# Performance work log

Hardware: AMD Instinct MI355X
Metric: run time of the kernel (lower is better)

The kernel has to match this reference:

```python
import jax, jax.numpy as jnp
import numpy as np

INPUT_DIM, LATENT_DIM, HIDDEN_DIM = 256, 128, 256
B, S = 1024, 256


def _linear_params(key, fan_in, fan_out):
    kw, kb = jax.random.split(key)
    scale = 1.0 / np.sqrt(fan_in)
    W = jax.random.uniform(kw, (fan_in, fan_out), jnp.float32, -scale, scale)
    b = jax.random.uniform(kb, (fan_out,), jnp.float32, -scale, scale)
    return W, b


def setup_inputs() -> dict:
    key = jax.random.key(0)
    ks = jax.random.split(key, 9)
    enc = jax.random.normal(ks[0], (B, S, INPUT_DIM), jnp.float32)
    prev_latent = jax.random.normal(ks[1], (B, LATENT_DIM), jnp.float32)
    eps = jax.random.normal(ks[2], (B, S, LATENT_DIM), jnp.float32)
    pW1, pb1 = _linear_params(ks[3], INPUT_DIM + LATENT_DIM, HIDDEN_DIM)
    pW2, pb2 = _linear_params(ks[4], HIDDEN_DIM, HIDDEN_DIM)
    pW3, pb3 = _linear_params(ks[5], HIDDEN_DIM, 2 * LATENT_DIM)
    qW1, qb1 = _linear_params(ks[6], 2 * INPUT_DIM + LATENT_DIM, HIDDEN_DIM)
    qW2, qb2 = _linear_params(ks[7], HIDDEN_DIM, HIDDEN_DIM)
    qW3, qb3 = _linear_params(ks[8], HIDDEN_DIM, 2 * LATENT_DIM)
    return {
        "encoder_features": enc, "prev_latent": prev_latent, "eps": eps,
        "pW1": pW1, "pb1": pb1, "pW2": pW2, "pb2": pb2, "pW3": pW3, "pb3": pb3,
        "qW1": qW1, "qb1": qb1, "qW2": qW2, "qb2": qb2, "qW3": qW3, "qb3": qb3,
    }


def _mlp3(x, W1, b1, W2, b2, W3, b3):
    h = jax.nn.relu(x @ W1 + b1)
    h = jax.nn.relu(h @ W2 + b2)
    return h @ W3 + b3


def reference(encoder_features, prev_latent, eps,
              pW1, pb1, pW2, pb2, pW3, pb3,
              qW1, qb1, qW2, qb2, qW3, qb3):
    # time-major for scan: [S, B, D]
    h_seq = jnp.swapaxes(encoder_features, 0, 1)
    e_seq = jnp.swapaxes(eps, 0, 1)

    def step(z, xs):
        h_t, e_t = xs  # [B, input_dim], [B, latent_dim]
        prior_out = _mlp3(jnp.concatenate([h_t, z], -1), pW1, pb1, pW2, pb2, pW3, pb3)
        pm, plv = jnp.split(prior_out, 2, axis=-1)
        post_out = _mlp3(jnp.concatenate([h_t, z, h_t], -1), qW1, qb1, qW2, qb2, qW3, qb3)
        qm, qlv = jnp.split(post_out, 2, axis=-1)
        z_t = qm + e_t * jnp.exp(0.5 * qlv)  # reparameterization
        return z_t, (z_t, pm, plv, qm, qlv)

    _, (z, pm, plv, qm, qlv) = jax.lax.scan(step, prev_latent, (h_seq, e_seq))
    # back to batch-major [B, S, latent_dim]
    tb = lambda a: jnp.swapaxes(a, 0, 1)
    return tb(z), tb(pm), tb(plv), tb(qm), tb(qlv)
```

## Files before the change

### kernel.cpp

```cpp
#include <hip/hip_runtime.h>


typedef __attribute__((ext_vector_type(8))) short bfrag8;
typedef __attribute__((ext_vector_type(4))) float facc4;
typedef __attribute__((ext_vector_type(4))) unsigned int u32x4;

__device__ __forceinline__ unsigned short f2bf(float x) {
  unsigned int u = __float_as_uint(x);
  u = (u + 0x7fffu + ((u >> 16) & 1u)) >> 16;
  return (unsigned short)u;
}
__device__ __forceinline__ unsigned int pk2(float a, float b) {
  return (unsigned int)f2bf(a) | ((unsigned int)f2bf(b) << 16);
}
__device__ __forceinline__ float bf2f(unsigned int lo) {
  return __uint_as_float(lo << 16);
}
__device__ __forceinline__ facc4 mfma_bf16(bfrag8 a, bfrag8 b, facc4 c) {
  return __builtin_amdgcn_mfma_f32_16x16x32_bf16(a, b, c, 0, 0, 0);
}
__device__ __forceinline__ bfrag8 load_pin(const unsigned short* p) {
  u32x4 v = *(const u32x4*)p;
  asm volatile("" : "+v"(v));
  return __builtin_bit_cast(bfrag8, v);
}
__device__ __forceinline__ void wg_barrier() {
  asm volatile("s_waitcnt lgkmcnt(0)" ::: "memory");
  __builtin_amdgcn_sched_barrier(0);
  __builtin_amdgcn_s_barrier();
  __builtin_amdgcn_sched_barrier(0);
}
#define SWC(r, c) ((c) ^ (((r) & 8) << 1))

__global__ void pack_all(const float* __restrict__ qW1, const float* __restrict__ qW2,
                         const float* __restrict__ qW3, const float* __restrict__ pW1,
                         const float* __restrict__ pW2, const float* __restrict__ pW3,
                         unsigned short* __restrict__ ws) {
  int b = blockIdx.x;
  const float* src; const float* src2 = nullptr; unsigned short* dst; int KT;
  if (b < 32)       { src = qW1; src2 = qW1 + 384 * 256; dst = ws;          KT = 8; }
  else if (b < 48)  { b -= 32;  src = qW1 + 256 * 256;   dst = ws + 65536;  KT = 4; }
  else if (b < 80)  { b -= 48;  src = qW2;               dst = ws + 98304;  KT = 8; }
  else if (b < 112) { b -= 80;  src = qW3;               dst = ws + 163840; KT = 8; }
  else if (b < 144) { b -= 112; src = pW1;               dst = ws + 229376; KT = 8; }
  else if (b < 160) { b -= 144; src = pW1 + 256 * 256;   dst = ws + 294912; KT = 4; }
  else if (b < 192) { b -= 160; src = pW2;               dst = ws + 327680; KT = 8; }
  else              { b -= 192; src = pW3;               dst = ws + 393216; KT = 8; }
  int t = b * 256 + (int)threadIdx.x;
  if (t >= 16 * KT * 64) return;
  int l  = t & 63;
  int kt = (t >> 6) % KT;
  int nt = t / (64 * KT);
  int n  = nt * 16 + (l & 15);
  int k0 = kt * 32 + (l >> 4) * 8;
  unsigned int o[4];
#pragma unroll
  for (int p = 0; p < 4; ++p) {
    float a = src[(size_t)(k0 + 2 * p) * 256 + n];
    float c = src[(size_t)(k0 + 2 * p + 1) * 256 + n];
    if (src2) {
      a += src2[(size_t)(k0 + 2 * p) * 256 + n];
      c += src2[(size_t)(k0 + 2 * p + 1) * 256 + n];
    }
    o[p] = pk2(a, c);
  }
  *(uint4*)(dst + (size_t)t * 8) = make_uint4(o[0], o[1], o[2], o[3]);
}

__global__ __launch_bounds__(256, 2) void k1_pre(
    const float* __restrict__ enc, const unsigned short* __restrict__ wq,
    const unsigned short* __restrict__ wp, const float* __restrict__ qb1,
    unsigned short* __restrict__ cq, unsigned short* __restrict__ cp) {
  __shared__ unsigned short xl[32 * 264];
  const int bid = blockIdx.x;
  const int gp = bid >> 8, s = bid & 255;
  const int tid = threadIdx.x;
  {
    int row = tid >> 3, c0 = (tid & 7) * 32;
    const float* sp = enc + (((size_t)(gp * 32 + row) * 256 + s) * 256 + c0);
#pragma unroll
    for (int q = 0; q < 4; ++q) {
      float4 a = *(const float4*)(sp + q * 8);
      float4 b = *(const float4*)(sp + q * 8 + 4);
      *(uint4*)(&xl[row * 264 + SWC(row, c0 + q * 8)]) =
          make_uint4(pk2(a.x, a.y), pk2(a.z, a.w), pk2(b.x, b.y), pk2(b.z, b.w));
    }
  }
  __syncthreads();
  const int w = tid >> 6, l = tid & 63, lm = l & 15, lg = l >> 4;
  const int rr = lg * 4;
  const int nt[4] = {2 * w, 2 * w + 1, 2 * w + 8, 2 * w + 9};
  facc4 aq[2][4], ap[2][4];
#pragma unroll
  for (int j = 0; j < 4; ++j) {
    float bv = qb1[nt[j] * 16 + lm];
    aq[0][j] = (facc4){bv, bv, bv, bv}; aq[1][j] = aq[0][j];
    ap[0][j] = (facc4){0.f, 0.f, 0.f, 0.f}; ap[1][j] = ap[0][j];
  }
#pragma unroll
  for (int kt = 0; kt < 8; ++kt) {
    bfrag8 bq[4], bp[4];
#pragma unroll
    for (int j = 0; j < 4; ++j) {
      bq[j] = *(const bfrag8*)(wq + ((size_t)(nt[j] * 8 + kt) * 64 + l) * 8);
      bp[j] = *(const bfrag8*)(wp + ((size_t)(nt[j] * 8 + kt) * 64 + l) * 8);
    }
#pragma unroll
    for (int rt = 0; rt < 2; ++rt) {
      bfrag8 x = *(const bfrag8*)(&xl[(rt * 16 + lm) * 264 + SWC(lm, kt * 32 + lg * 8)]);
#pragma unroll
      for (int j = 0; j < 4; ++j) {
        aq[rt][j] = mfma_bf16(x, bq[j], aq[rt][j]);
        ap[rt][j] = mfma_bf16(x, bp[j], ap[rt][j]);
      }
    }
  }
#pragma unroll
  for (int rt = 0; rt < 2; ++rt) {
    size_t base = ((size_t)((gp * 2 + rt) * 256 + s)) * 512 + (size_t)tid * 2;
    ((uint4*)cq)[base + 0] =
        make_uint4(pk2(aq[rt][0][0], aq[rt][0][1]), pk2(aq[rt][0][2], aq[rt][0][3]),
                   pk2(aq[rt][2][0], aq[rt][2][1]), pk2(aq[rt][2][2], aq[rt][2][3]));
    ((uint4*)cq)[base + 1] =
        make_uint4(pk2(aq[rt][1][0], aq[rt][1][1]), pk2(aq[rt][1][2], aq[rt][1][3]),
                   pk2(aq[rt][3][0], aq[rt][3][1]), pk2(aq[rt][3][2], aq[rt][3][3]));
#pragma unroll
    for (int i = 0; i < 4; ++i) {
      int b = gp * 32 + rt * 16 + rr + i;
      ((uint2*)cp)[((size_t)b * 256 + s) * 64 + w * 16 + lm] =
          make_uint2(pk2(ap[rt][0][i], ap[rt][1][i]), pk2(ap[rt][2][i], ap[rt][3][i]));
    }
  }
}

__global__ __launch_bounds__(512, 2) void k2_scan(
    const float* __restrict__ prevz, const float* __restrict__ eps,
    const unsigned short* __restrict__ wU, const unsigned short* __restrict__ wW2,
    const unsigned short* __restrict__ wW3,
    const float* __restrict__ qb2, const float* __restrict__ qb3,
    const unsigned short* __restrict__ cq,
    float* __restrict__ z_o, float* __restrict__ qm_o, float* __restrict__ qlv_o) {
  __shared__ unsigned short zl[16 * 136];
  __shared__ unsigned short h1[16 * 264];
  __shared__ unsigned short h2[16 * 264];
  const int g = blockIdx.x, tid = threadIdx.x;
  const int w = tid >> 6, l = tid & 63, lm = l & 15, lg = l >> 4;
  const int rr = lg * 4;
  const int c = 16 * w + lm;
  const int cc[2] = {c, 128 + c};

  bfrag8 u[2][4], w2[2][8], w3[2][8];
#pragma unroll
  for (int j = 0; j < 2; ++j) {
    const int nt = w + 8 * j;
#pragma unroll
    for (int kt = 0; kt < 4; ++kt)
      u[j][kt] = load_pin(wU + ((size_t)(nt * 4 + kt) * 64 + l) * 8);
#pragma unroll
    for (int kt = 0; kt < 8; ++kt) {
      w2[j][kt] = load_pin(wW2 + ((size_t)(nt * 8 + kt) * 64 + l) * 8);
      w3[j][kt] = load_pin(wW3 + ((size_t)(nt * 8 + kt) * 64 + l) * 8);
    }
  }
  const float b2[2] = {qb2[c], qb2[128 + c]};
  const float b3[2] = {qb3[c], qb3[128 + c]};
  {
    int row = tid >> 5, q0 = (tid & 31) * 4;
    float4 v = *(const float4*)(prevz + (size_t)(g * 16 + row) * 128 + q0);
    *(uint2*)(&zl[row * 136 + SWC(row, q0)]) = make_uint2(pk2(v.x, v.y), pk2(v.z, v.w));
  }
  const uint4* cqp = (const uint4*)cq + ((size_t)g * 256) * 512 +
                     (size_t)((w >> 1) * 64 + l) * 2 + (w & 1);
  uint4 cb = cqp[0];
  float ep[4];
#pragma unroll
  for (int i = 0; i < 4; ++i)
    ep[i] = eps[((size_t)(g * 16 + rr + i) * 256) * 128 + c];
  __syncthreads();

  for (int s = 0; s < 256; ++s) {
    facc4 a[2];
    a[0][0] = bf2f(cb.x & 0xffffu); a[0][1] = bf2f(cb.x >> 16);
    a[0][2] = bf2f(cb.y & 0xffffu); a[0][3] = bf2f(cb.y >> 16);
    a[1][0] = bf2f(cb.z & 0xffffu); a[1][1] = bf2f(cb.z >> 16);
    a[1][2] = bf2f(cb.w & 0xffffu); a[1][3] = bf2f(cb.w >> 16);
    const int sn = (s + 1 < 256) ? s + 1 : s;
    const uint4 nb = cqp[(size_t)sn * 512];
    float epn[4];
#pragma unroll
    for (int i = 0; i < 4; ++i)
      epn[i] = eps[((size_t)(g * 16 + rr + i) * 256 + sn) * 128 + c];
#pragma unroll
    for (int kt = 0; kt < 4; ++kt) {
      bfrag8 zf = *(const bfrag8*)(&zl[lm * 136 + SWC(lm, kt * 32 + lg * 8)]);
      a[0] = mfma_bf16(zf, u[0][kt], a[0]);
      a[1] = mfma_bf16(zf, u[1][kt], a[1]);
    }
#pragma unroll
    for (int j = 0; j < 2; ++j)
#pragma unroll
      for (int i = 0; i < 4; ++i)
        h1[(rr + i) * 264 + SWC(rr + i, cc[j])] = f2bf(fmaxf(a[j][i], 0.f));
    wg_barrier();
    facc4 cv[2] = {(facc4){b2[0], b2[0], b2[0], b2[0]},
                   (facc4){b2[1], b2[1], b2[1], b2[1]}};
#pragma unroll
    for (int kt = 0; kt < 8; ++kt) {
      bfrag8 hf = *(const bfrag8*)(&h1[lm * 264 + SWC(lm, kt * 32 + lg * 8)]);
      cv[0] = mfma_bf16(hf, w2[0][kt], cv[0]);
      cv[1] = mfma_bf16(hf, w2[1][kt], cv[1]);
    }
#pragma unroll
    for (int j = 0; j < 2; ++j)
#pragma unroll
      for (int i = 0; i < 4; ++i)
        h2[(rr + i) * 264 + SWC(rr + i, cc[j])] = f2bf(fmaxf(cv[j][i], 0.f));
    wg_barrier();
    facc4 o[2] = {(facc4){b3[0], b3[0], b3[0], b3[0]},
                  (facc4){b3[1], b3[1], b3[1], b3[1]}};
#pragma unroll
    for (int kt = 0; kt < 8; ++kt) {
      bfrag8 hf = *(const bfrag8*)(&h2[lm * 264 + SWC(lm, kt * 32 + lg * 8)]);
      o[0] = mfma_bf16(hf, w3[0][kt], o[0]);
      o[1] = mfma_bf16(hf, w3[1][kt], o[1]);
    }
#pragma unroll
    for (int i = 0; i < 4; ++i) {
      size_t ob = ((size_t)(g * 16 + rr + i) * 256 + s) * 128;
      float zq = o[0][i] + ep[i] * __expf(0.5f * o[1][i]);
      qm_o[ob + c]  = o[0][i];
      qlv_o[ob + c] = o[1][i];
      z_o[ob + c]   = zq;
      zl[(rr + i) * 136 + SWC(rr + i, c)] = f2bf(zq);
    }
    wg_barrier();
    cb = nb;
#pragma unroll
    for (int i = 0; i < 4; ++i) ep[i] = epn[i];
  }
}

__global__ __launch_bounds__(256, 2) void k3_prior(
    const float* __restrict__ prevz, const float* __restrict__ z_in,
    const unsigned short* __restrict__ cp,
    const unsigned short* __restrict__ wU, const unsigned short* __restrict__ w2p,
    const unsigned short* __restrict__ w3p,
    const float* __restrict__ pb1, const float* __restrict__ pb2,
    const float* __restrict__ pb3,
    float* __restrict__ pm_o, float* __restrict__ plv_o) {
  __shared__ unsigned short zl[64 * 136];
  __shared__ unsigned short hb[64 * 264];
  const int bid = blockIdx.x;
  const int gp = bid >> 8, s = bid & 255;
  const int tid = threadIdx.x;
  const int w = tid >> 6, l = tid & 63, lm = l & 15, lg = l >> 4;
  const int rr = lg * 4;
  const int nt[4] = {2 * w, 2 * w + 1, 2 * w + 8, 2 * w + 9};
  const int c0 = 32 * w + lm, c1 = c0 + 16;
  const int cc[4] = {c0, c1, 128 + c0, 128 + c1};
  {
    int row = tid >> 2, q0 = (tid & 3) * 32;
    const float* sp = (s == 0) ? (prevz + (size_t)(gp * 64 + row) * 128 + q0)
                               : (z_in + ((size_t)(gp * 64 + row) * 256 + (s - 1)) * 128 + q0);
#pragma unroll
    for (int q = 0; q < 4; ++q) {
      float4 a = *(const float4*)(sp + q * 8);
      float4 b = *(const float4*)(sp + q * 8 + 4);
      *(uint4*)(&zl[row * 136 + SWC(row, q0 + q * 8)]) =
          make_uint4(pk2(a.x, a.y), pk2(a.z, a.w), pk2(b.x, b.y), pk2(b.z, b.w));
    }
  }
  const float pb[4] = {pb1[nt[0] * 16 + lm], pb1[nt[1] * 16 + lm],
                       pb1[nt[2] * 16 + lm], pb1[nt[3] * 16 + lm]};
  facc4 acc[4][4];
#pragma unroll
  for (int rt = 0; rt < 4; ++rt)
#pragma unroll
    for (int i = 0; i < 4; ++i) {
      int b = gp * 64 + rt * 16 + rr + i;
      uint2 v = ((const uint2*)cp)[((size_t)b * 256 + s) * 64 + w * 16 + lm];
      acc[rt][0][i] = pb[0] + bf2f(v.x & 0xffffu);
      acc[rt][1][i] = pb[1] + bf2f(v.x >> 16);
      acc[rt][2][i] = pb[2] + bf2f(v.y & 0xffffu);
      acc[rt][3][i] = pb[3] + bf2f(v.y >> 16);
    }
  __syncthreads();
#pragma unroll
  for (int kt = 0; kt < 4; ++kt) {
    bfrag8 b0 = *(const bfrag8*)(wU + ((size_t)(nt[0] * 4 + kt) * 64 + l) * 8);
    bfrag8 b1 = *(const bfrag8*)(wU + ((size_t)(nt[1] * 4 + kt) * 64 + l) * 8);
    bfrag8 b2f = *(const bfrag8*)(wU + ((size_t)(nt[2] * 4 + kt) * 64 + l) * 8);
    bfrag8 b3f = *(const bfrag8*)(wU + ((size_t)(nt[3] * 4 + kt) * 64 + l) * 8);
#pragma unroll
    for (int rt = 0; rt < 4; ++rt) {
      bfrag8 zf = *(const bfrag8*)(&zl[(rt * 16 + lm) * 136 + SWC(lm, kt * 32 + lg * 8)]);
      acc[rt][0] = mfma_bf16(zf, b0, acc[rt][0]);
      acc[rt][1] = mfma_bf16(zf, b1, acc[rt][1]);
      acc[rt][2] = mfma_bf16(zf, b2f, acc[rt][2]);
      acc[rt][3] = mfma_bf16(zf, b3f, acc[rt][3]);
    }
  }
#pragma unroll
  for (int rt = 0; rt < 4; ++rt)
#pragma unroll
    for (int j = 0; j < 4; ++j)
#pragma unroll
      for (int i = 0; i < 4; ++i) {
        int r = rt * 16 + rr + i;
        hb[r * 264 + SWC(r, cc[j])] = f2bf(fmaxf(acc[rt][j][i], 0.f));
      }
  __syncthreads();
  facc4 a2[4][4];
#pragma unroll
  for (int rt = 0; rt < 4; ++rt)
#pragma unroll
    for (int j = 0; j < 4; ++j) a2[rt][j] = (facc4){pb2[nt[j] * 16 + lm], pb2[nt[j] * 16 + lm],
                                                    pb2[nt[j] * 16 + lm], pb2[nt[j] * 16 + lm]};
#pragma unroll
  for (int kt = 0; kt < 8; ++kt) {
    bfrag8 b0 = *(const bfrag8*)(w2p + ((size_t)(nt[0] * 8 + kt) * 64 + l) * 8);
    bfrag8 b1 = *(const bfrag8*)(w2p + ((size_t)(nt[1] * 8 + kt) * 64 + l) * 8);
    bfrag8 b2f = *(const bfrag8*)(w2p + ((size_t)(nt[2] * 8 + kt) * 64 + l) * 8);
    bfrag8 b3f = *(const bfrag8*)(w2p + ((size_t)(nt[3] * 8 + kt) * 64 + l) * 8);
#pragma unroll
    for (int rt = 0; rt < 4; ++rt) {
      bfrag8 hf = *(const bfrag8*)(&hb[(rt * 16 + lm) * 264 + SWC(lm, kt * 32 + lg * 8)]);
      a2[rt][0] = mfma_bf16(hf, b0, a2[rt][0]);
      a2[rt][1] = mfma_bf16(hf, b1, a2[rt][1]);
      a2[rt][2] = mfma_bf16(hf, b2f, a2[rt][2]);
      a2[rt][3] = mfma_bf16(hf, b3f, a2[rt][3]);
    }
  }
  __syncthreads();
#pragma unroll
  for (int rt = 0; rt < 4; ++rt)
#pragma unroll
    for (int j = 0; j < 4; ++j)
#pragma unroll
      for (int i = 0; i < 4; ++i) {
        int r = rt * 16 + rr + i;
        hb[r * 264 + SWC(r, cc[j])] = f2bf(fmaxf(a2[rt][j][i], 0.f));
      }
  __syncthreads();
  facc4 a3[4][4];
#pragma unroll
  for (int rt = 0; rt < 4; ++rt)
#pragma unroll
    for (int j = 0; j < 4; ++j) a3[rt][j] = (facc4){pb3[nt[j] * 16 + lm], pb3[nt[j] * 16 + lm],
                                                    pb3[nt[j] * 16 + lm], pb3[nt[j] * 16 + lm]};
#pragma unroll
  for (int kt = 0; kt < 8; ++kt) {
    bfrag8 b0 = *(const bfrag8*)(w3p + ((size_t)(nt[0] * 8 + kt) * 64 + l) * 8);
    bfrag8 b1 = *(const bfrag8*)(w3p + ((size_t)(nt[1] * 8 + kt) * 64 + l) * 8);
    bfrag8 b2f = *(const bfrag8*)(w3p + ((size_t)(nt[2] * 8 + kt) * 64 + l) * 8);
    bfrag8 b3f = *(const bfrag8*)(w3p + ((size_t)(nt[3] * 8 + kt) * 64 + l) * 8);
#pragma unroll
    for (int rt = 0; rt < 4; ++rt) {
      bfrag8 hf = *(const bfrag8*)(&hb[(rt * 16 + lm) * 264 + SWC(lm, kt * 32 + lg * 8)]);
      a3[rt][0] = mfma_bf16(hf, b0, a3[rt][0]);
      a3[rt][1] = mfma_bf16(hf, b1, a3[rt][1]);
      a3[rt][2] = mfma_bf16(hf, b2f, a3[rt][2]);
      a3[rt][3] = mfma_bf16(hf, b3f, a3[rt][3]);
    }
  }
#pragma unroll
  for (int rt = 0; rt < 4; ++rt)
#pragma unroll
    for (int i = 0; i < 4; ++i) {
      size_t base = ((size_t)(gp * 64 + rt * 16 + rr + i) * 256 + s) * 128;
      pm_o[base + c0]  = a3[rt][0][i];
      pm_o[base + c1]  = a3[rt][1][i];
      plv_o[base + c0] = a3[rt][2][i];
      plv_o[base + c1] = a3[rt][3][i];
    }
}

extern "C" void kernel_launch(void* const* d_in, const int* in_sizes, int n_in,
                              void* d_out, int out_size, void* d_ws, size_t ws_size,
                              hipStream_t stream) {
  const float* enc   = (const float*)d_in[0];
  const float* prevz = (const float*)d_in[1];
  const float* eps   = (const float*)d_in[2];
  const float* pW1 = (const float*)d_in[3];
  const float* pb1 = (const float*)d_in[4];
  const float* pW2 = (const float*)d_in[5];
  const float* pb2 = (const float*)d_in[6];
  const float* pW3 = (const float*)d_in[7];
  const float* pb3 = (const float*)d_in[8];
  const float* qW1 = (const float*)d_in[9];
  const float* qb1 = (const float*)d_in[10];
  const float* qW2 = (const float*)d_in[11];
  const float* qb2 = (const float*)d_in[12];
  const float* qW3 = (const float*)d_in[13];
  const float* qb3 = (const float*)d_in[14];

  float* out = (float*)d_out;
  const size_t O = (size_t)1024 * 256 * 128;
  float* z_o   = out;
  float* pm_o  = out + O;
  float* plv_o = out + 2 * O;
  float* qm_o  = out + 3 * O;
  float* qlv_o = out + 4 * O;
  unsigned short* cq = (unsigned short*)pm_o;
  unsigned short* cp = (unsigned short*)plv_o;

  unsigned short* ws = (unsigned short*)d_ws;
  unsigned short* Wqe  = ws;
  unsigned short* Uq   = ws + 65536;
  unsigned short* W2q  = ws + 98304;
  unsigned short* W3q  = ws + 163840;
  unsigned short* W1ph = ws + 229376;
  unsigned short* Up   = ws + 294912;
  unsigned short* W2p  = ws + 327680;
  unsigned short* W3p  = ws + 393216;

  pack_all<<<224, 256, 0, stream>>>(qW1, qW2, qW3, pW1, pW2, pW3, ws);
  k1_pre<<<8192, 256, 0, stream>>>(enc, Wqe, W1ph, qb1, cq, cp);
  k2_scan<<<64, 512, 0, stream>>>(prevz, eps, Uq, W2q, W3q, qb2, qb3, cq,
                                  z_o, qm_o, qlv_o);
  k3_prior<<<4096, 256, 0, stream>>>(prevz, z_o, cp, Up, W2p, W3p,
                                     pb1, pb2, pb3, pm_o, plv_o);
}
```

Measured before the change: 755.8 us.

## Fuse pre, scan and prior kernels into one persistent kernel with flag sync

```diff
diff --git a/kernel.cpp b/kernel.cpp
--- a/kernel.cpp
+++ b/kernel.cpp
@@ -4,6 +4,9 @@
 typedef __attribute__((ext_vector_type(8))) short bfrag8;
 typedef __attribute__((ext_vector_type(4))) float facc4;
 typedef __attribute__((ext_vector_type(4))) unsigned int u32x4;
+typedef unsigned long long ull;
+
+#define SCOPE_AGENT __HIP_MEMORY_SCOPE_AGENT
 
 __device__ __forceinline__ unsigned short f2bf(float x) {
   unsigned int u = __float_as_uint(x);
@@ -67,14 +70,12 @@
   *(uint4*)(dst + (size_t)t * 8) = make_uint4(o[0], o[1], o[2], o[3]);
 }
 
-__global__ __launch_bounds__(256, 2) void k1_pre(
+template<bool FUSED>
+__device__ __forceinline__ void k1_body(
+    int gp, int s, int tid, unsigned short* xl,
     const float* __restrict__ enc, const unsigned short* __restrict__ wq,
     const unsigned short* __restrict__ wp, const float* __restrict__ qb1,
-    unsigned short* __restrict__ cq, unsigned short* __restrict__ cp) {
-  __shared__ unsigned short xl[32 * 264];
-  const int bid = blockIdx.x;
-  const int gp = bid >> 8, s = bid & 255;
-  const int tid = threadIdx.x;
+    unsigned int* __restrict__ cq, unsigned short* __restrict__ cp) {
   {
     int row = tid >> 3, c0 = (tid & 7) * 32;
     const float* sp = enc + (((size_t)(gp * 32 + row) * 256 + s) * 256 + c0);
@@ -117,33 +118,38 @@
   }
 #pragma unroll
   for (int rt = 0; rt < 2; ++rt) {
-    size_t base = ((size_t)((gp * 2 + rt) * 256 + s)) * 512 + (size_t)tid * 2;
-    ((uint4*)cq)[base + 0] =
-        make_uint4(pk2(aq[rt][0][0], aq[rt][0][1]), pk2(aq[rt][0][2], aq[rt][0][3]),
-                   pk2(aq[rt][2][0], aq[rt][2][1]), pk2(aq[rt][2][2], aq[rt][2][3]));
-    ((uint4*)cq)[base + 1] =
-        make_uint4(pk2(aq[rt][1][0], aq[rt][1][1]), pk2(aq[rt][1][2], aq[rt][1][3]),
-                   pk2(aq[rt][3][0], aq[rt][3][1]), pk2(aq[rt][3][2], aq[rt][3][3]));
 #pragma unroll
     for (int i = 0; i < 4; ++i) {
       int b = gp * 32 + rt * 16 + rr + i;
-      ((uint2*)cp)[((size_t)b * 256 + s) * 64 + w * 16 + lm] =
-          make_uint2(pk2(ap[rt][0][i], ap[rt][1][i]), pk2(ap[rt][2][i], ap[rt][3][i]));
-    }
-  }
-}
-
-__global__ __launch_bounds__(512, 2) void k2_scan(
+      size_t rb = ((size_t)b * 256 + s) * 128;
+      unsigned int v0 = pk2(aq[rt][0][i], aq[rt][2][i]);
+      unsigned int v1 = pk2(aq[rt][1][i], aq[rt][3][i]);
+      ull vcp = (ull)pk2(ap[rt][0][i], ap[rt][1][i]) |
+                ((ull)pk2(ap[rt][2][i], ap[rt][3][i]) << 32);
+      size_t cpx = ((size_t)b * 256 + s) * 64 + w * 16 + lm;
+      if (FUSED) {
+        __hip_atomic_store(cq + rb + 32 * w + lm,      v0, __ATOMIC_RELAXED, SCOPE_AGENT);
+        __hip_atomic_store(cq + rb + 32 * w + 16 + lm, v1, __ATOMIC_RELAXED, SCOPE_AGENT);
+        __hip_atomic_store((ull*)cp + cpx, vcp, __ATOMIC_RELAXED, SCOPE_AGENT);
+      } else {
+        cq[rb + 32 * w + lm]      = v0;
+        cq[rb + 32 * w + 16 + lm] = v1;
+        ((ull*)cp)[cpx] = vcp;
+      }
+    }
+  }
+}
+
+template<bool FUSED>
+__device__ __forceinline__ void k2_body(
+    int g, int tid, unsigned short* zl, unsigned short* h1, unsigned short* h2,
     const float* __restrict__ prevz, const float* __restrict__ eps,
     const unsigned short* __restrict__ wU, const unsigned short* __restrict__ wW2,
     const unsigned short* __restrict__ wW3,
     const float* __restrict__ qb2, const float* __restrict__ qb3,
-    const unsigned short* __restrict__ cq,
-    float* __restrict__ z_o, float* __restrict__ qm_o, float* __restrict__ qlv_o) {
-  __shared__ unsigned short zl[16 * 136];
-  __shared__ unsigned short h1[16 * 264];
-  __shared__ unsigned short h2[16 * 264];
-  const int g = blockIdx.x, tid = threadIdx.x;
+    const unsigned int* __restrict__ cq,
+    float* __restrict__ z_o, float* __restrict__ qm_o, float* __restrict__ qlv_o,
+    int* cqflag, int* zdone) {
   const int w = tid >> 6, l = tid & 63, lm = l & 15, lg = l >> 4;
   const int rr = lg * 4;
   const int c = 16 * w + lm;
@@ -169,77 +175,326 @@
     float4 v = *(const float4*)(prevz + (size_t)(g * 16 + row) * 128 + q0);
     *(uint2*)(&zl[row * 136 + SWC(row, q0)]) = make_uint2(pk2(v.x, v.y), pk2(v.z, v.w));
   }
-  const uint4* cqp = (const uint4*)cq + ((size_t)g * 256) * 512 +
-                     (size_t)((w >> 1) * 64 + l) * 2 + (w & 1);
-  uint4 cb = cqp[0];
+  if (FUSED) {
+    if (tid == 0)
+      while (__hip_atomic_load(&cqflag[0], __ATOMIC_ACQUIRE, SCOPE_AGENT) < 32)
+        __builtin_amdgcn_s_sleep(2);
+    wg_barrier();
+  }
+  size_t rix[4];
+#pragma unroll
+  for (int i = 0; i < 4; ++i)
+    rix[i] = ((size_t)(g * 16 + rr + i) * 256) * 128 + c;
+  unsigned int cb[4];
+#pragma unroll
+  for (int i = 0; i < 4; ++i) cb[i] = cq[rix[i]];
   float ep[4];
 #pragma unroll
   for (int i = 0; i < 4; ++i)
     ep[i] = eps[((size_t)(g * 16 + rr + i) * 256) * 128 + c];
   __syncthreads();
 
-  for (int s = 0; s < 256; ++s) {
-    facc4 a[2];
-    a[0][0] = bf2f(cb.x & 0xffffu); a[0][1] = bf2f(cb.x >> 16);
-    a[0][2] = bf2f(cb.y & 0xffffu); a[0][3] = bf2f(cb.y >> 16);
-    a[1][0] = bf2f(cb.z & 0xffffu); a[1][1] = bf2f(cb.z >> 16);
-    a[1][2] = bf2f(cb.w & 0xffffu); a[1][3] = bf2f(cb.w >> 16);
-    const int sn = (s + 1 < 256) ? s + 1 : s;
-    const uint4 nb = cqp[(size_t)sn * 512];
-    float epn[4];
-#pragma unroll
-    for (int i = 0; i < 4; ++i)
-      epn[i] = eps[((size_t)(g * 16 + rr + i) * 256 + sn) * 128 + c];
-#pragma unroll
-    for (int kt = 0; kt < 4; ++kt) {
-      bfrag8 zf = *(const bfrag8*)(&zl[lm * 136 + SWC(lm, kt * 32 + lg * 8)]);
-      a[0] = mfma_bf16(zf, u[0][kt], a[0]);
-      a[1] = mfma_bf16(zf, u[1][kt], a[1]);
-    }
-#pragma unroll
-    for (int j = 0; j < 2; ++j)
+  for (int sb = 0; sb < 32; ++sb) {
+    if (FUSED) {
+      if (sb > 0 && l == 0)
+        __hip_atomic_fetch_add(&zdone[g], 1, __ATOMIC_RELEASE, SCOPE_AGENT);
+      if (tid == 0) {
+        int hi = sb * 8 + 8; if (hi > 255) hi = 255;
+        for (int q = sb * 8 + 1; q <= hi; ++q)
+          while (__hip_atomic_load(&cqflag[q], __ATOMIC_ACQUIRE, SCOPE_AGENT) < 32)
+            __builtin_amdgcn_s_sleep(2);
+      }
+      wg_barrier();
+    }
+#pragma unroll 1
+    for (int si = 0; si < 8; ++si) {
+      const int s = sb * 8 + si;
+      facc4 a[2];
+#pragma unroll
+      for (int i = 0; i < 4; ++i) {
+        a[0][i] = bf2f(cb[i] & 0xffffu);
+        a[1][i] = bf2f(cb[i] >> 16);
+      }
+      const int sn = (s + 1 < 256) ? s + 1 : s;
+      unsigned int nbv[4];
+#pragma unroll
+      for (int i = 0; i < 4; ++i) nbv[i] = cq[rix[i] + (size_t)sn * 128];
+      float epn[4];
 #pragma unroll
       for (int i = 0; i < 4; ++i)
-        h1[(rr + i) * 264 + SWC(rr + i, cc[j])] = f2bf(fmaxf(a[j][i], 0.f));
-    wg_barrier();
-    facc4 cv[2] = {(facc4){b2[0], b2[0], b2[0], b2[0]},
-                   (facc4){b2[1], b2[1], b2[1], b2[1]}};
-#pragma unroll
-    for (int kt = 0; kt < 8; ++kt) {
-      bfrag8 hf = *(const bfrag8*)(&h1[lm * 264 + SWC(lm, kt * 32 + lg * 8)]);
-      cv[0] = mfma_bf16(hf, w2[0][kt], cv[0]);
-      cv[1] = mfma_bf16(hf, w2[1][kt], cv[1]);
-    }
-#pragma unroll
-    for (int j = 0; j < 2; ++j)
-#pragma unroll
-      for (int i = 0; i < 4; ++i)
-        h2[(rr + i) * 264 + SWC(rr + i, cc[j])] = f2bf(fmaxf(cv[j][i], 0.f));
-    wg_barrier();
-    facc4 o[2] = {(facc4){b3[0], b3[0], b3[0], b3[0]},
-                  (facc4){b3[1], b3[1], b3[1], b3[1]}};
-#pragma unroll
-    for (int kt = 0; kt < 8; ++kt) {
-      bfrag8 hf = *(const bfrag8*)(&h2[lm * 264 + SWC(lm, kt * 32 + lg * 8)]);
-      o[0] = mfma_bf16(hf, w3[0][kt], o[0]);
-      o[1] = mfma_bf16(hf, w3[1][kt], o[1]);
-    }
+        epn[i] = eps[((size_t)(g * 16 + rr + i) * 256 + sn) * 128 + c];
+#pragma unroll
+      for (int kt = 0; kt < 4; ++kt) {
+        bfrag8 zf = *(const bfrag8*)(&zl[lm * 136 + SWC(lm, kt * 32 + lg * 8)]);
+        a[0] = mfma_bf16(zf, u[0][kt], a[0]);
+        a[1] = mfma_bf16(zf, u[1][kt], a[1]);
+      }
+#pragma unroll
+      for (int j = 0; j < 2; ++j)
+#pragma unroll
+        for (int i = 0; i < 4; ++i)
+          h1[(rr + i) * 264 + SWC(rr + i, cc[j])] = f2bf(fmaxf(a[j][i], 0.f));
+      wg_barrier();
+      facc4 cv[2] = {(facc4){b2[0], b2[0], b2[0], b2[0]},
+                     (facc4){b2[1], b2[1], b2[1], b2[1]}};
+#pragma unroll
+      for (int kt = 0; kt < 8; ++kt) {
+        bfrag8 hf = *(const bfrag8*)(&h1[lm * 264 + SWC(lm, kt * 32 + lg * 8)]);
+        cv[0] = mfma_bf16(hf, w2[0][kt], cv[0]);
+        cv[1] = mfma_bf16(hf, w2[1][kt], cv[1]);
+      }
+#pragma unroll
+      for (int j = 0; j < 2; ++j)
+#pragma unroll
+        for (int i = 0; i < 4; ++i)
+          h2[(rr + i) * 264 + SWC(rr + i, cc[j])] = f2bf(fmaxf(cv[j][i], 0.f));
+      wg_barrier();
+      facc4 o[2] = {(facc4){b3[0], b3[0], b3[0], b3[0]},
+                    (facc4){b3[1], b3[1], b3[1], b3[1]}};
+#pragma unroll
+      for (int kt = 0; kt < 8; ++kt) {
+        bfrag8 hf = *(const bfrag8*)(&h2[lm * 264 + SWC(lm, kt * 32 + lg * 8)]);
+        o[0] = mfma_bf16(hf, w3[0][kt], o[0]);
+        o[1] = mfma_bf16(hf, w3[1][kt], o[1]);
+      }
+#pragma unroll
+      for (int i = 0; i < 4; ++i) {
+        size_t ob = ((size_t)(g * 16 + rr + i) * 256 + s) * 128;
+        float zq = o[0][i] + ep[i] * __expf(0.5f * o[1][i]);
+        qm_o[ob + c]  = o[0][i];
+        qlv_o[ob + c] = o[1][i];
+        if (FUSED)
+          __hip_atomic_store(&z_o[ob + c], zq, __ATOMIC_RELAXED, SCOPE_AGENT);
+        else
+          z_o[ob + c] = zq;
+        zl[(rr + i) * 136 + SWC(rr + i, c)] = f2bf(zq);
+      }
+      wg_barrier();
+#pragma unroll
+      for (int i = 0; i < 4; ++i) { cb[i] = nbv[i]; ep[i] = epn[i]; }
+    }
+  }
+  if (FUSED) {
+    asm volatile("s_waitcnt vmcnt(0)" ::: "memory");
+    if (l == 0)
+      __hip_atomic_fetch_add(&zdone[g], 1, __ATOMIC_RELEASE, SCOPE_AGENT);
+  }
+}
+
+template<bool FUSED>
+__device__ __forceinline__ void k3_body(
+    int gp, int s, int tid, unsigned short* zl, unsigned short* hb,
+    const float* __restrict__ prevz, const float* __restrict__ z_in,
+    const unsigned short* __restrict__ cp,
+    const unsigned short* __restrict__ wU, const unsigned short* __restrict__ w2p,
+    const unsigned short* __restrict__ w3p,
+    const float* __restrict__ pb1, const float* __restrict__ pb2,
+    const float* __restrict__ pb3,
+    float* __restrict__ pm_o, float* __restrict__ plv_o,
+    int* cqflag, int* zdone) {
+  if (FUSED) {
+    if (tid == 0) {
+      while (__hip_atomic_load(&cqflag[s], __ATOMIC_ACQUIRE, SCOPE_AGENT) < 32)
+        __builtin_amdgcn_s_sleep(8);
+      int need = 8 * ((s + 7) >> 3);
+      if (need) {
+#pragma unroll
+        for (int j = 0; j < 4; ++j)
+          while (__hip_atomic_load(&zdone[4 * gp + j], __ATOMIC_ACQUIRE, SCOPE_AGENT) < need)
+            __builtin_amdgcn_s_sleep(8);
+      }
+    }
+    __syncthreads();
+  }
+  const int w = tid >> 6, l = tid & 63, lm = l & 15, lg = l >> 4;
+  const int rr = lg * 4;
+  const int nt[4] = {2 * w, 2 * w + 1, 2 * w + 8, 2 * w + 9};
+  const int c0 = 32 * w + lm, c1 = c0 + 16;
+  const int cc[4] = {c0, c1, 128 + c0, 128 + c1};
+  {
+    int row = tid >> 2, q0 = (tid & 3) * 32;
+    const float* sp = (s == 0) ? (prevz + (size_t)(gp * 64 + row) * 128 + q0)
+                               : (z_in + ((size_t)(gp * 64 + row) * 256 + (s - 1)) * 128 + q0);
+#pragma unroll
+    for (int q = 0; q < 4; ++q) {
+      float4 a = *(const float4*)(sp + q * 8);
+      float4 b = *(const float4*)(sp + q * 8 + 4);
+      *(uint4*)(&zl[row * 136 + SWC(row, q0 + q * 8)]) =
+          make_uint4(pk2(a.x, a.y), pk2(a.z, a.w), pk2(b.x, b.y), pk2(b.z, b.w));
+    }
+  }
+  const float pb[4] = {pb1[nt[0] * 16 + lm], pb1[nt[1] * 16 + lm],
+                       pb1[nt[2] * 16 + lm], pb1[nt[3] * 16 + lm]};
+  facc4 acc[4][4];
+#pragma unroll
+  for (int rt = 0; rt < 4; ++rt)
 #pragma unroll
     for (int i = 0; i < 4; ++i) {
-      size_t ob = ((size_t)(g * 16 + rr + i) * 256 + s) * 128;
-      float zq = o[0][i] + ep[i] * __expf(0.5f * o[1][i]);
-      qm_o[ob + c]  = o[0][i];
-      qlv_o[ob + c] = o[1][i];
-      z_o[ob + c]   = zq;
-      zl[(rr + i) * 136 + SWC(rr + i, c)] = f2bf(zq);
-    }
-    wg_barrier();
-    cb = nb;
-#pragma unroll
-    for (int i = 0; i < 4; ++i) ep[i] = epn[i];
-  }
-}
-
+      int b = gp * 64 + rt * 16 + rr + i;
+      ull v = ((const ull*)cp)[((size_t)b * 256 + s) * 64 + w * 16 + lm];
+      unsigned int vx = (unsigned int)v, vy = (unsigned int)(v >> 32);
+      acc[rt][0][i] = pb[0] + bf2f(vx & 0xffffu);
+      acc[rt][1][i] = pb[1] + bf2f(vx >> 16);
+      acc[rt][2][i] = pb[2] + bf2f(vy & 0xffffu);
+      acc[rt][3][i] = pb[3] + bf2f(vy >> 16);
+    }
+  __syncthreads();
+#pragma unroll
+  for (int kt = 0; kt < 4; ++kt) {
+    bfrag8 b0 = *(const bfrag8*)(wU + ((size_t)(nt[0] * 4 + kt) * 64 + l) * 8);
+    bfrag8 b1 = *(const bfrag8*)(wU + ((size_t)(nt[1] * 4 + kt) * 64 + l) * 8);
+    bfrag8 b2f = *(const bfrag8*)(wU + ((size_t)(nt[2] * 4 + kt) * 64 + l) * 8);
+    bfrag8 b3f = *(const bfrag8*)(wU + ((size_t)(nt[3] * 4 + kt) * 64 + l) * 8);
+#pragma unroll
+    for (int rt = 0; rt < 4; ++rt) {
+      bfrag8 zf = *(const bfrag8*)(&zl[(rt * 16 + lm) * 136 + SWC(lm, kt * 32 + lg * 8)]);
+      acc[rt][0] = mfma_bf16(zf, b0, acc[rt][0]);
+      acc[rt][1] = mfma_bf16(zf, b1, acc[rt][1]);
+      acc[rt][2] = mfma_bf16(zf, b2f, acc[rt][2]);
+      acc[rt][3] = mfma_bf16(zf, b3f, acc[rt][3]);
+    }
+  }
+#pragma unroll
+  for (int rt = 0; rt < 4; ++rt)
+#pragma unroll
+    for (int j = 0; j < 4; ++j)
+#pragma unroll
+      for (int i = 0; i < 4; ++i) {
+        int r = rt * 16 + rr + i;
+        hb[r * 264 + SWC(r, cc[j])] = f2bf(fmaxf(acc[rt][j][i], 0.f));
+      }
+  __syncthreads();
+  facc4 a2[4][4];
+#pragma unroll
+  for (int rt = 0; rt < 4; ++rt)
+#pragma unroll
+    for (int j = 0; j < 4; ++j) a2[rt][j] = (facc4){pb2[nt[j] * 16 + lm], pb2[nt[j] * 16 + lm],
+                                                    pb2[nt[j] * 16 + lm], pb2[nt[j] * 16 + lm]};
+#pragma unroll
+  for (int kt = 0; kt < 8; ++kt) {
+    bfrag8 b0 = *(const bfrag8*)(w2p + ((size_t)(nt[0] * 8 + kt) * 64 + l) * 8);
+    bfrag8 b1 = *(const bfrag8*)(w2p + ((size_t)(nt[1] * 8 + kt) * 64 + l) * 8);
+    bfrag8 b2f = *(const bfrag8*)(w2p + ((size_t)(nt[2] * 8 + kt) * 64 + l) * 8);
+    bfrag8 b3f = *(const bfrag8*)(w2p + ((size_t)(nt[3] * 8 + kt) * 64 + l) * 8);
+#pragma unroll
+    for (int rt = 0; rt < 4; ++rt) {
+      bfrag8 hf = *(const bfrag8*)(&hb[(rt * 16 + lm) * 264 + SWC(lm, kt * 32 + lg * 8)]);
+      a2[rt][0] = mfma_bf16(hf, b0, a2[rt][0]);
+      a2[rt][1] = mfma_bf16(hf, b1, a2[rt][1]);
+      a2[rt][2] = mfma_bf16(hf, b2f, a2[rt][2]);
+      a2[rt][3] = mfma_bf16(hf, b3f, a2[rt][3]);
+    }
+  }
+  __syncthreads();
+#pragma unroll
+  for (int rt = 0; rt < 4; ++rt)
+#pragma unroll
+    for (int j = 0; j < 4; ++j)
+#pragma unroll
+      for (int i = 0; i < 4; ++i) {
+        int r = rt * 16 + rr + i;
+        hb[r * 264 + SWC(r, cc[j])] = f2bf(fmaxf(a2[rt][j][i], 0.f));
+      }
+  __syncthreads();
+  facc4 a3[4][4];
+#pragma unroll
+  for (int rt = 0; rt < 4; ++rt)
+#pragma unroll
+    for (int j = 0; j < 4; ++j) a3[rt][j] = (facc4){pb3[nt[j] * 16 + lm], pb3[nt[j] * 16 + lm],
+                                                    pb3[nt[j] * 16 + lm], pb3[nt[j] * 16 + lm]};
+#pragma unroll
+  for (int kt = 0; kt < 8; ++kt) {
+    bfrag8 b0 = *(const bfrag8*)(w3p + ((size_t)(nt[0] * 8 + kt) * 64 + l) * 8);
+    bfrag8 b1 = *(const bfrag8*)(w3p + ((size_t)(nt[1] * 8 + kt) * 64 + l) * 8);
+    bfrag8 b2f = *(const bfrag8*)(w3p + ((size_t)(nt[2] * 8 + kt) * 64 + l) * 8);
+    bfrag8 b3f = *(const bfrag8*)(w3p + ((size_t)(nt[3] * 8 + kt) * 64 + l) * 8);
+#pragma unroll
+    for (int rt = 0; rt < 4; ++rt) {
+      bfrag8 hf = *(const bfrag8*)(&hb[(rt * 16 + lm) * 264 + SWC(lm, kt * 32 + lg * 8)]);
+      a3[rt][0] = mfma_bf16(hf, b0, a3[rt][0]);
+      a3[rt][1] = mfma_bf16(hf, b1, a3[rt][1]);
+      a3[rt][2] = mfma_bf16(hf, b2f, a3[rt][2]);
+      a3[rt][3] = mfma_bf16(hf, b3f, a3[rt][3]);
+    }
+  }
+#pragma unroll
+  for (int rt = 0; rt < 4; ++rt)
+#pragma unroll
+    for (int i = 0; i < 4; ++i) {
+      size_t base = ((size_t)(gp * 64 + rt * 16 + rr + i) * 256 + s) * 128;
+      pm_o[base + c0]  = a3[rt][0][i];
+      pm_o[base + c1]  = a3[rt][1][i];
+      plv_o[base + c0] = a3[rt][2][i];
+      plv_o[base + c1] = a3[rt][3][i];
+    }
+}
+
+__global__ __launch_bounds__(512, 2) void mega(
+    const float* __restrict__ enc, const float* __restrict__ prevz,
+    const float* __restrict__ eps,
+    const unsigned short* __restrict__ Wqe, const unsigned short* __restrict__ Uq,
+    const unsigned short* __restrict__ W2q, const unsigned short* __restrict__ W3q,
+    const unsigned short* __restrict__ W1ph, const unsigned short* __restrict__ Up,
+    const unsigned short* __restrict__ W2p, const unsigned short* __restrict__ W3p,
+    const float* __restrict__ qb1, const float* __restrict__ qb2,
+    const float* __restrict__ qb3, const float* __restrict__ pb1,
+    const float* __restrict__ pb2, const float* __restrict__ pb3,
+    unsigned int* cq, unsigned short* cp,
+    float* z_o, float* qm_o, float* qlv_o, float* pm_o, float* plv_o,
+    int* cqflag, int* zdone) {
+  __shared__ __align__(16) char smem[51200];
+  const int bid = blockIdx.x;
+  const int tid = threadIdx.x;
+  if (bid < 4096) {
+    const int spair = bid >> 5, gp = bid & 31;
+    const int h = tid >> 8, t = tid & 255;
+    const int s = 2 * spair + h;
+    unsigned short* xl = (unsigned short*)smem + h * (32 * 264);
+    k1_body<true>(gp, s, t, xl, enc, Wqe, W1ph, qb1, cq, cp);
+    __syncthreads();
+    if (tid == 0) {
+      __hip_atomic_fetch_add(&cqflag[2 * spair],     1, __ATOMIC_RELEASE, SCOPE_AGENT);
+      __hip_atomic_fetch_add(&cqflag[2 * spair + 1], 1, __ATOMIC_RELEASE, SCOPE_AGENT);
+    }
+  } else if (bid < 4160) {
+    const int g = bid - 4096;
+    unsigned short* zl = (unsigned short*)smem;
+    unsigned short* h1 = zl + 16 * 136;
+    unsigned short* h2 = h1 + 16 * 264;
+    k2_body<true>(g, tid, zl, h1, h2, prevz, eps, Uq, W2q, W3q, qb2, qb3, cq,
+                  z_o, qm_o, qlv_o, cqflag, zdone);
+  } else {
+    if (tid >= 256) return;
+    const int b2 = bid - 4160;
+    const int s = b2 >> 4, gp = b2 & 15;
+    unsigned short* zl = (unsigned short*)smem;
+    unsigned short* hb = zl + 64 * 136;
+    k3_body<true>(gp, s, tid, zl, hb, prevz, z_o, cp, Up, W2p, W3p,
+                  pb1, pb2, pb3, pm_o, plv_o, cqflag, zdone);
+  }
+}
+
+__global__ __launch_bounds__(256, 2) void k1_pre(
+    const float* __restrict__ enc, const unsigned short* __restrict__ wq,
+    const unsigned short* __restrict__ wp, const float* __restrict__ qb1,
+    unsigned int* __restrict__ cq, unsigned short* __restrict__ cp) {
+  __shared__ unsigned short xl[32 * 264];
+  k1_body<false>(blockIdx.x >> 8, blockIdx.x & 255, threadIdx.x, xl,
+                 enc, wq, wp, qb1, cq, cp);
+}
+__global__ __launch_bounds__(512, 2) void k2_scan(
+    const float* __restrict__ prevz, const float* __restrict__ eps,
+    const unsigned short* __restrict__ wU, const unsigned short* __restrict__ wW2,
+    const unsigned short* __restrict__ wW3,
+    const float* __restrict__ qb2, const float* __restrict__ qb3,
+    const unsigned int* __restrict__ cq,
+    float* __restrict__ z_o, float* __restrict__ qm_o, float* __restrict__ qlv_o) {
+  __shared__ unsigned short zl[16 * 136];
+  __shared__ unsigned short h1[16 * 264];
+  __shared__ unsigned short h2[16 * 264];
+  k2_body<false>(blockIdx.x, threadIdx.x, zl, h1, h2, prevz, eps, wU, wW2, wW3,
+                 qb2, qb3, cq, z_o, qm_o, qlv_o, nullptr, nullptr);
+}
 __global__ __launch_bounds__(256, 2) void k3_prior(
     const float* __restrict__ prevz, const float* __restrict__ z_in,
     const unsigned short* __restrict__ cp,
@@ -250,129 +505,9 @@
     float* __restrict__ pm_o, float* __restrict__ plv_o) {
   __shared__ unsigned short zl[64 * 136];
   __shared__ unsigned short hb[64 * 264];
-  const int bid = blockIdx.x;
-  const int gp = bid >> 8, s = bid & 255;
-  const int tid = threadIdx.x;
-  const int w = tid >> 6, l = tid & 63, lm = l & 15, lg = l >> 4;
-  const int rr = lg * 4;
-  const int nt[4] = {2 * w, 2 * w + 1, 2 * w + 8, 2 * w + 9};
-  const int c0 = 32 * w + lm, c1 = c0 + 16;
-  const int cc[4] = {c0, c1, 128 + c0, 128 + c1};
-  {
-    int row = tid >> 2, q0 = (tid & 3) * 32;
-    const float* sp = (s == 0) ? (prevz + (size_t)(gp * 64 + row) * 128 + q0)
-                               : (z_in + ((size_t)(gp * 64 + row) * 256 + (s - 1)) * 128 + q0);
-#pragma unroll
-    for (int q = 0; q < 4; ++q) {
-      float4 a = *(const float4*)(sp + q * 8);
-      float4 b = *(const float4*)(sp + q * 8 + 4);
-      *(uint4*)(&zl[row * 136 + SWC(row, q0 + q * 8)]) =
-          make_uint4(pk2(a.x, a.y), pk2(a.z, a.w), pk2(b.x, b.y), pk2(b.z, b.w));
-    }
-  }
-  const float pb[4] = {pb1[nt[0] * 16 + lm], pb1[nt[1] * 16 + lm],
-                       pb1[nt[2] * 16 + lm], pb1[nt[3] * 16 + lm]};
-  facc4 acc[4][4];
-#pragma unroll
-  for (int rt = 0; rt < 4; ++rt)
-#pragma unroll
-    for (int i = 0; i < 4; ++i) {
-      int b = gp * 64 + rt * 16 + rr + i;
-      uint2 v = ((const uint2*)cp)[((size_t)b * 256 + s) * 64 + w * 16 + lm];
-      acc[rt][0][i] = pb[0] + bf2f(v.x & 0xffffu);
-      acc[rt][1][i] = pb[1] + bf2f(v.x >> 16);
-      acc[rt][2][i] = pb[2] + bf2f(v.y & 0xffffu);
-      acc[rt][3][i] = pb[3] + bf2f(v.y >> 16);
-    }
-  __syncthreads();
-#pragma unroll
-  for (int kt = 0; kt < 4; ++kt) {
-    bfrag8 b0 = *(const bfrag8*)(wU + ((size_t)(nt[0] * 4 + kt) * 64 + l) * 8);
-    bfrag8 b1 = *(const bfrag8*)(wU + ((size_t)(nt[1] * 4 + kt) * 64 + l) * 8);
-    bfrag8 b2f = *(const bfrag8*)(wU + ((size_t)(nt[2] * 4 + kt) * 64 + l) * 8);
-    bfrag8 b3f = *(const bfrag8*)(wU + ((size_t)(nt[3] * 4 + kt) * 64 + l) * 8);
-#pragma unroll
-    for (int rt = 0; rt < 4; ++rt) {
-      bfrag8 zf = *(const bfrag8*)(&zl[(rt * 16 + lm) * 136 + SWC(lm, kt * 32 + lg * 8)]);
-      acc[rt][0] = mfma_bf16(zf, b0, acc[rt][0]);
-      acc[rt][1] = mfma_bf16(zf, b1, acc[rt][1]);
-      acc[rt][2] = mfma_bf16(zf, b2f, acc[rt][2]);
-      acc[rt][3] = mfma_bf16(zf, b3f, acc[rt][3]);
-    }
-  }
-#pragma unroll
-  for (int rt = 0; rt < 4; ++rt)
-#pragma unroll
-    for (int j = 0; j < 4; ++j)
-#pragma unroll
-      for (int i = 0; i < 4; ++i) {
-        int r = rt * 16 + rr + i;
-        hb[r * 264 + SWC(r, cc[j])] = f2bf(fmaxf(acc[rt][j][i], 0.f));
-      }
-  __syncthreads();
-  facc4 a2[4][4];
-#pragma unroll
-  for (int rt = 0; rt < 4; ++rt)
-#pragma unroll
-    for (int j = 0; j < 4; ++j) a2[rt][j] = (facc4){pb2[nt[j] * 16 + lm], pb2[nt[j] * 16 + lm],
-                                                    pb2[nt[j] * 16 + lm], pb2[nt[j] * 16 + lm]};
-#pragma unroll
-  for (int kt = 0; kt < 8; ++kt) {
-    bfrag8 b0 = *(const bfrag8*)(w2p + ((size_t)(nt[0] * 8 + kt) * 64 + l) * 8);
-    bfrag8 b1 = *(const bfrag8*)(w2p + ((size_t)(nt[1] * 8 + kt) * 64 + l) * 8);
-    bfrag8 b2f = *(const bfrag8*)(w2p + ((size_t)(nt[2] * 8 + kt) * 64 + l) * 8);
-    bfrag8 b3f = *(const bfrag8*)(w2p + ((size_t)(nt[3] * 8 + kt) * 64 + l) * 8);
-#pragma unroll
-    for (int rt = 0; rt < 4; ++rt) {
-      bfrag8 hf = *(const bfrag8*)(&hb[(rt * 16 + lm) * 264 + SWC(lm, kt * 32 + lg * 8)]);
-      a2[rt][0] = mfma_bf16(hf, b0, a2[rt][0]);
-      a2[rt][1] = mfma_bf16(hf, b1, a2[rt][1]);
-      a2[rt][2] = mfma_bf16(hf, b2f, a2[rt][2]);
-      a2[rt][3] = mfma_bf16(hf, b3f, a2[rt][3]);
-    }
-  }
-  __syncthreads();
-#pragma unroll
-  for (int rt = 0; rt < 4; ++rt)
-#pragma unroll
-    for (int j = 0; j < 4; ++j)
-#pragma unroll
-      for (int i = 0; i < 4; ++i) {
-        int r = rt * 16 + rr + i;
-        hb[r * 264 + SWC(r, cc[j])] = f2bf(fmaxf(a2[rt][j][i], 0.f));
-      }
-  __syncthreads();
-  facc4 a3[4][4];
-#pragma unroll
-  for (int rt = 0; rt < 4; ++rt)
-#pragma unroll
-    for (int j = 0; j < 4; ++j) a3[rt][j] = (facc4){pb3[nt[j] * 16 + lm], pb3[nt[j] * 16 + lm],
-                                                    pb3[nt[j] * 16 + lm], pb3[nt[j] * 16 + lm]};
-#pragma unroll
-  for (int kt = 0; kt < 8; ++kt) {
-    bfrag8 b0 = *(const bfrag8*)(w3p + ((size_t)(nt[0] * 8 + kt) * 64 + l) * 8);
-    bfrag8 b1 = *(const bfrag8*)(w3p + ((size_t)(nt[1] * 8 + kt) * 64 + l) * 8);
-    bfrag8 b2f = *(const bfrag8*)(w3p + ((size_t)(nt[2] * 8 + kt) * 64 + l) * 8);
-    bfrag8 b3f = *(const bfrag8*)(w3p + ((size_t)(nt[3] * 8 + kt) * 64 + l) * 8);
-#pragma unroll
-    for (int rt = 0; rt < 4; ++rt) {
-      bfrag8 hf = *(const bfrag8*)(&hb[(rt * 16 + lm) * 264 + SWC(lm, kt * 32 + lg * 8)]);
-      a3[rt][0] = mfma_bf16(hf, b0, a3[rt][0]);
-      a3[rt][1] = mfma_bf16(hf, b1, a3[rt][1]);
-      a3[rt][2] = mfma_bf16(hf, b2f, a3[rt][2]);
-      a3[rt][3] = mfma_bf16(hf, b3f, a3[rt][3]);
-    }
-  }
-#pragma unroll
-  for (int rt = 0; rt < 4; ++rt)
-#pragma unroll
-    for (int i = 0; i < 4; ++i) {
-      size_t base = ((size_t)(gp * 64 + rt * 16 + rr + i) * 256 + s) * 128;
-      pm_o[base + c0]  = a3[rt][0][i];
-      pm_o[base + c1]  = a3[rt][1][i];
-      plv_o[base + c0] = a3[rt][2][i];
-      plv_o[base + c1] = a3[rt][3][i];
-    }
+  k3_body<false>(blockIdx.x >> 8, blockIdx.x & 255, threadIdx.x, zl, hb,
+                 prevz, z_in, cp, wU, w2p, w3p, pb1, pb2, pb3, pm_o, plv_o,
+                 nullptr, nullptr);
 }
 
 extern "C" void kernel_launch(void* const* d_in, const int* in_sizes, int n_in,
@@ -401,7 +536,7 @@
   float* plv_o = out + 2 * O;
   float* qm_o  = out + 3 * O;
   float* qlv_o = out + 4 * O;
-  unsigned short* cq = (unsigned short*)pm_o;
+  unsigned int*   cq = (unsigned int*)qm_o;
   unsigned short* cp = (unsigned short*)plv_o;
 
   unsigned short* ws = (unsigned short*)d_ws;
@@ -414,10 +549,24 @@
   unsigned short* W2p  = ws + 327680;
   unsigned short* W3p  = ws + 393216;
 
+  const size_t FLAGS_OFF = 458752u * 2u;
+  int* cqflag = (int*)((char*)d_ws + FLAGS_OFF);
+  int* zdone  = cqflag + 256;
+  const bool fused = ws_size >= FLAGS_OFF + 320 * sizeof(int);
+
   pack_all<<<224, 256, 0, stream>>>(qW1, qW2, qW3, pW1, pW2, pW3, ws);
-  k1_pre<<<8192, 256, 0, stream>>>(enc, Wqe, W1ph, qb1, cq, cp);
-  k2_scan<<<64, 512, 0, stream>>>(prevz, eps, Uq, W2q, W3q, qb2, qb3, cq,
-                                  z_o, qm_o, qlv_o);
-  k3_prior<<<4096, 256, 0, stream>>>(prevz, z_o, cp, Up, W2p, W3p,
-                                     pb1, pb2, pb3, pm_o, plv_o);
-}
+  if (fused) {
+    hipMemsetAsync(cqflag, 0, 320 * sizeof(int), stream);
+    mega<<<8256, 512, 0, stream>>>(enc, prevz, eps,
+                                   Wqe, Uq, W2q, W3q, W1ph, Up, W2p, W3p,
+                                   qb1, qb2, qb3, pb1, pb2, pb3,
+                                   cq, cp, z_o, qm_o, qlv_o, pm_o, plv_o,
+                                   cqflag, zdone);
+  } else {
+    k1_pre<<<8192, 256, 0, stream>>>(enc, Wqe, W1ph, qb1, cq, cp);
+    k2_scan<<<64, 512, 0, stream>>>(prevz, eps, Uq, W2q, W3q, qb2, qb3, cq,
+                                    z_o, qm_o, qlv_o);
+    k3_prior<<<4096, 256, 0, stream>>>(prevz, z_o, cp, Up, W2p, W3p,
+                                       pb1, pb2, pb3, pm_o, plv_o);
+  }
+}
```

Result: slower. 2.290 ms (+203.0%).
